# Kernel tuning notes

Hardware: AMD Instinct MI355X
Metric: run time of the kernel (lower is better)

Reference implementation:

```python
import jax, jax.numpy as jnp
import numpy as np

EMBED_DIM = 768
NUM_HEADS = 12
HEAD_DIM = EMBED_DIM // NUM_HEADS
SCALING = HEAD_DIM ** -0.5


def setup_inputs() -> dict:
    key = jax.random.key(0)
    ks = jax.random.split(key, 12)
    B, S, E, H = 4, 1024, EMBED_DIM, NUM_HEADS
    inp = {
        "hidden_states": jax.random.normal(ks[0], (B, S, E), dtype=jnp.float32),
        "pos_row": jax.random.randint(ks[1], (B, S), 0, 64, dtype=jnp.int32),
        "pos_col": jax.random.randint(ks[2], (B, S), 0, 32, dtype=jnp.int32),
        "q_w": jax.random.normal(ks[3], (E, E), dtype=jnp.float32) * 0.02,
        "q_b": jnp.zeros((E,), dtype=jnp.float32),
        "k_w": jax.random.normal(ks[4], (E, E), dtype=jnp.float32) * 0.02,
        "k_b": jnp.zeros((E,), dtype=jnp.float32),
        "v_w": jax.random.normal(ks[5], (E, E), dtype=jnp.float32) * 0.02,
        "v_b": jnp.zeros((E,), dtype=jnp.float32),
        "o_w": jax.random.normal(ks[6], (E, E), dtype=jnp.float32) * 0.02,
        "o_b": jnp.zeros((E,), dtype=jnp.float32),
        "rel_table": jax.random.normal(ks[7], (4, H), dtype=jnp.float32) * 0.02,
    }
    return inp


def _generate_bias(pos_row, pos_col, rel_table):
    # relative row/col differences: [B, S, S]
    rel_row = pos_row[:, :, None] - pos_row[:, None, :]
    rel_col = pos_col[:, :, None] - pos_col[:, None, :]
    rel_cell = jnp.abs(rel_row) + jnp.abs(rel_col)
    # table index: other=0, same row=1, same col=2, same cell=3 (priority order as in torch code)
    idx = jnp.where(rel_row == 0, 1, 0)
    idx = jnp.where(rel_col == 0, 2, idx)
    idx = jnp.where(rel_cell == 0, 3, idx)
    # gather: [B, S, S, H] -> [B, H, S, S]
    bias = rel_table[idx]
    return jnp.transpose(bias, (0, 3, 1, 2))


def reference(hidden_states, pos_row, pos_col, q_w, q_b, k_w, k_b, v_w, v_b, o_w, o_b, rel_table):
    B, S, E = hidden_states.shape
    H, D = NUM_HEADS, HEAD_DIM

    def shape(x):  # [B, S, E] -> [B, H, S, D]
        return jnp.transpose(x.reshape(B, S, H, D), (0, 2, 1, 3))

    q = shape((hidden_states @ q_w.T + q_b) * SCALING)
    k = shape(hidden_states @ k_w.T + k_b)
    v = shape(hidden_states @ v_w.T + v_b)

    # [B, H, S, S]
    attn = jnp.einsum("bhqd,bhkd->bhqk", q, k)
    attn = attn + _generate_bias(pos_row, pos_col, rel_table)
    attn = jax.nn.softmax(attn, axis=-1)

    out = jnp.einsum("bhqk,bhkd->bhqd", attn, v)  # [B, H, S, D]
    out = jnp.transpose(out, (0, 2, 1, 3)).reshape(B, S, E)
    return out @ o_w.T + o_b
```

## Files before the change

### kernel.cpp

```cpp
#include <hip/hip_runtime.h>

#define NHEADS 12
#define HDIM   64
#define EMB    768
#define SEQ    1024
#define BATCH  4
#define MTOT   (BATCH * SEQ)

typedef __bf16 bf16x8 __attribute__((ext_vector_type(8)));
typedef float  f32x4  __attribute__((ext_vector_type(4)));

#define GLB(p) ((const __attribute__((address_space(1))) uint32_t*)(p))
#define LDS(p) ((__attribute__((address_space(3))) uint32_t*)(p))

__device__ __forceinline__ uint bfr(float f) {
    uint u = __float_as_uint(f);
    return (u + 0x7fffu + ((u >> 16) & 1u)) >> 16;
}

__global__ __launch_bounds__(256) void split_f32(
    const float* __restrict__ x, ushort* __restrict__ hi,
    ushort* __restrict__ lo, int n4)
{
    int i = blockIdx.x * 256 + threadIdx.x;
    if (i >= n4) return;
    float4 v = ((const float4*)x)[i];
    float f[4] = {v.x, v.y, v.z, v.w};
    ushort hh[4], ll[4];
#pragma unroll
    for (int j = 0; j < 4; ++j) {
        uint h = bfr(f[j]);
        float hf = __uint_as_float(h << 16);
        ll[j] = (ushort)bfr(f[j] - hf);
        hh[j] = (ushort)h;
    }
    ushort4 hv = {hh[0], hh[1], hh[2], hh[3]};
    ushort4 lv = {ll[0], ll[1], ll[2], ll[3]};
    ((ushort4*)hi)[i] = hv;
    ((ushort4*)lo)[i] = lv;
}

template <int MODE>
__global__ __launch_bounds__(256) void gemm_mfma(
    const ushort* __restrict__ Ah, const ushort* __restrict__ Al,
    const ushort* __restrict__ Wh, const ushort* __restrict__ Wl,
    const float* __restrict__ b0, const float* __restrict__ b1,
    const float* __restrict__ b2,
    ushort* __restrict__ q16, ushort* __restrict__ k16,
    ushort* __restrict__ vT16, float* __restrict__ o0)
{
    __shared__ __align__(16) ushort lds_buf[16384];
    char* ldsc = (char*)lds_buf;

    const int t  = threadIdx.x;
    const int w  = t >> 6;
    const int l  = t & 63;
    const int m0 = blockIdx.x * 128;
    const int n0 = blockIdx.y * 128;
    const int wm = w >> 1;
    const int wn = w & 1;

    const int soff0 = w * 1024 + l * 16;
    const int soff1 = soff0 + 4096;
    const int srow0 = soff0 >> 6, srow1 = soff1 >> 6;
    const int ss0 = (((soff0 >> 4) & 3) ^ ((srow0 >> 1) & 3));
    const int ss1 = (((soff1 >> 4) & 3) ^ ((srow1 >> 1) & 3));

    const char* gb[4] = {
        (const char*)Ah + (size_t)m0 * 1536,
        (const char*)Al + (size_t)m0 * 1536,
        (const char*)Wh + (size_t)n0 * 1536,
        (const char*)Wl + (size_t)n0 * 1536};
    const size_t go0 = (size_t)srow0 * 1536 + ss0 * 16;
    const size_t go1 = (size_t)srow1 * 1536 + ss1 * 16;
    const int ldsu0 = w * 1024;
    const int ldsu1 = w * 1024 + 4096;

    int aoff[4], boff[4];
#pragma unroll
    for (int i = 0; i < 4; ++i) {
        int row = wm * 64 + i * 16 + (l & 15);
        aoff[i] = row * 64 + ((((l >> 4) ^ ((row >> 1) & 3))) << 4);
        int rn = wn * 64 + i * 16 + (l & 15);
        boff[i] = rn * 64 + ((((l >> 4) ^ ((rn >> 1) & 3))) << 4);
    }

    f32x4 acc[4][4] = {};

    for (int ks = 0; ks < 24; ++ks) {
        const size_t kb = (size_t)ks * 64;
        __syncthreads();
#pragma unroll
        for (int tt = 0; tt < 4; ++tt) {
            __builtin_amdgcn_global_load_lds(GLB(gb[tt] + go0 + kb),
                                             LDS(ldsc + tt * 8192 + ldsu0), 16, 0, 0);
            __builtin_amdgcn_global_load_lds(GLB(gb[tt] + go1 + kb),
                                             LDS(ldsc + tt * 8192 + ldsu1), 16, 0, 0);
        }
        __syncthreads();

        bf16x8 ah[4], al[4], bh[4], bl[4];
#pragma unroll
        for (int i = 0; i < 4; ++i) {
            ah[i] = *(const bf16x8*)(ldsc + aoff[i]);
            al[i] = *(const bf16x8*)(ldsc + 8192 + aoff[i]);
            bh[i] = *(const bf16x8*)(ldsc + 16384 + boff[i]);
            bl[i] = *(const bf16x8*)(ldsc + 24576 + boff[i]);
        }
#pragma unroll
        for (int i = 0; i < 4; ++i)
#pragma unroll
            for (int j = 0; j < 4; ++j) {
                acc[i][j] = __builtin_amdgcn_mfma_f32_16x16x32_bf16(ah[i], bh[j], acc[i][j], 0, 0, 0);
                acc[i][j] = __builtin_amdgcn_mfma_f32_16x16x32_bf16(ah[i], bl[j], acc[i][j], 0, 0, 0);
                acc[i][j] = __builtin_amdgcn_mfma_f32_16x16x32_bf16(al[i], bh[j], acc[i][j], 0, 0, 0);
            }
    }

    const int mrow_base = m0 + wm * 64 + ((l >> 4) << 2);

    if (MODE == 1) {
        const int which = (n0 >= 1536) ? 2 : (n0 >= 768 ? 1 : 0);
        const float* bp = (which == 0) ? b0 : (which == 1 ? b1 : b2);
        ushort* op = (which == 0) ? q16 : (which == 1 ? k16 : vT16);
        const float scale = (which == 0) ? 0.125f : 1.0f;
        const int nin_base = n0 - which * 768 + wn * 64 + (l & 15);
#pragma unroll
        for (int j = 0; j < 4; ++j) {
            const int n_in = nin_base + j * 16;
            const float bv = bp[n_in];
            const int h = n_in >> 6, d = n_in & 63;
#pragma unroll
            for (int i = 0; i < 4; ++i)
#pragma unroll
                for (int r = 0; r < 4; ++r) {
                    const int m = mrow_base + i * 16 + r;
                    const int bb = m >> 10, s = m & 1023;
                    const ushort u = (ushort)bfr((acc[i][j][r] + bv) * scale);
                    const size_t dst = (which == 2)
                        ? ((size_t)((bb * NHEADS + h) * HDIM + d) * SEQ + s)
                        : ((size_t)((bb * NHEADS + h) * SEQ + s) * HDIM + d);
                    op[dst] = u;
                }
        }
    } else {
        const int nin_base = n0 + wn * 64 + (l & 15);
#pragma unroll
        for (int j = 0; j < 4; ++j) {
            const int n_in = nin_base + j * 16;
            const float bv = b0[n_in];
#pragma unroll
            for (int i = 0; i < 4; ++i)
#pragma unroll
                for (int r = 0; r < 4; ++r) {
                    const int m = mrow_base + i * 16 + r;
                    o0[(size_t)m * 768 + n_in] = acc[i][j][r] + bv;
                }
        }
    }
}

#define QPOFF  0
#define KOFF   8192
#define VOFF   16384
#define POSOFF 24576

__global__ __launch_bounds__(256) void attn_mfma(
    const ushort* __restrict__ q16, const ushort* __restrict__ k16,
    const ushort* __restrict__ vT16, const int* __restrict__ pos_row,
    const int* __restrict__ pos_col, const float* __restrict__ rel_table,
    ushort* __restrict__ aoh, ushort* __restrict__ aol)
{
    __shared__ __align__(16) char lds[24832];

    const int t  = threadIdx.x;
    const int w  = t >> 6;
    const int l  = t & 63;
    const int bh = blockIdx.y;
    const int b  = bh / NHEADS;
    const int h  = bh - b * NHEADS;
    const int q0g = blockIdx.x * 64;

    const char* qb  = (const char*)(q16 + (size_t)bh * SEQ * HDIM);
    const char* kb  = (const char*)(k16 + (size_t)bh * SEQ * HDIM);
    const char* vtb = (const char*)(vT16 + (size_t)bh * HDIM * SEQ);

    const float t0 = rel_table[0 * NHEADS + h];
    const float t1 = rel_table[1 * NHEADS + h];
    const float t2 = rel_table[2 * NHEADS + h];
    const float t3 = rel_table[3 * NHEADS + h];

    const int o1 = t * 16, o2 = o1 + 4096;
    const int r1 = o1 >> 7, r2 = o2 >> 7;
    const int kq1 = o1 ^ ((r1 & 7) << 4);
    const int kq2 = o2 ^ ((r2 & 7) << 4);
    const int vs1 = r1 * 2048 + (((((o1 >> 4) & 7) ^ (r1 & 7))) << 4);
    const int vs2 = r2 * 2048 + (((((o2 >> 4) & 7) ^ (r2 & 7))) << 4);

    __builtin_amdgcn_global_load_lds(GLB(qb + (size_t)q0g * 128 + kq1),
                                     LDS(lds + QPOFF + w * 1024), 16, 0, 0);
    __builtin_amdgcn_global_load_lds(GLB(qb + (size_t)q0g * 128 + kq2),
                                     LDS(lds + QPOFF + w * 1024 + 4096), 16, 0, 0);

    const int qrow_g = q0g + w * 16 + (l & 15);
    const int pq = (pos_row[b * SEQ + qrow_g] << 8) | pos_col[b * SEQ + qrow_g];

    __syncthreads();

    bf16x8 qf[2];
    const int qrl = w * 16 + (l & 15);
#pragma unroll
    for (int ks = 0; ks < 2; ++ks)
        qf[ks] = *(const bf16x8*)(lds + QPOFF + qrl * 128 +
                                  ((((l >> 4) + 4 * ks) ^ (qrl & 7)) << 4));

    f32x4 pv[4] = {};
    float m_run = -1e30f, l_run = 0.0f;

    const int prow = l & 15;
    const int pswz = (prow & 7) << 4;
    const int pwbase = QPOFF + w * 2048 + prow * 128;

    for (int kt = 0; kt < 16; ++kt) {
        const int k0g = kt * 64;
        __syncthreads();
        __builtin_amdgcn_global_load_lds(GLB(kb + (size_t)k0g * 128 + kq1),
                                         LDS(lds + KOFF + w * 1024), 16, 0, 0);
        __builtin_amdgcn_global_load_lds(GLB(kb + (size_t)k0g * 128 + kq2),
                                         LDS(lds + KOFF + w * 1024 + 4096), 16, 0, 0);
        __builtin_amdgcn_global_load_lds(GLB(vtb + (size_t)k0g * 2 + vs1),
                                         LDS(lds + VOFF + w * 1024), 16, 0, 0);
        __builtin_amdgcn_global_load_lds(GLB(vtb + (size_t)k0g * 2 + vs2),
                                         LDS(lds + VOFF + w * 1024 + 4096), 16, 0, 0);
        if (t < 64) {
            int pr = pos_row[b * SEQ + k0g + t];
            int pc = pos_col[b * SEQ + k0g + t];
            *(int*)(lds + POSOFF + t * 4) = (pr << 8) | pc;
        }
        __syncthreads();

        f32x4 sacc[4] = {};
#pragma unroll
        for (int ks = 0; ks < 2; ++ks) {
            const bf16x8 qq = qf[ks];
#pragma unroll
            for (int j = 0; j < 4; ++j) {
                const int krow = j * 16 + (l & 15);
                const bf16x8 kf = *(const bf16x8*)(lds + KOFF + krow * 128 +
                                                   ((((l >> 4) + 4 * ks) ^ (krow & 7)) << 4));
                sacc[j] = __builtin_amdgcn_mfma_f32_16x16x32_bf16(kf, qq, sacc[j], 0, 0, 0);
            }
        }

        int4 pk4[4];
#pragma unroll
        for (int j = 0; j < 4; ++j)
            pk4[j] = *(const int4*)(lds + POSOFF + (l >> 4) * 16 + j * 64);

        float sv[16];
#pragma unroll
        for (int j = 0; j < 4; ++j) {
            const int pkk[4] = {pk4[j].x, pk4[j].y, pk4[j].z, pk4[j].w};
#pragma unroll
            for (int r = 0; r < 4; ++r) {
                const int dd = pq ^ pkk[r];
                const float bs = ((dd & 0xFF00) == 0)
                                     ? (((dd & 0xFF) == 0) ? t3 : t1)
                                     : (((dd & 0xFF) == 0) ? t2 : t0);
                sv[j * 4 + r] = sacc[j][r] + bs;
            }
        }
        float pm = sv[0];
#pragma unroll
        for (int i = 1; i < 16; ++i) pm = fmaxf(pm, sv[i]);
        pm = fmaxf(pm, __shfl_xor(pm, 16));
        pm = fmaxf(pm, __shfl_xor(pm, 32));
        const float mnew = fmaxf(m_run, pm);
        float psum = 0.0f;
#pragma unroll
        for (int i = 0; i < 16; ++i) {
            sv[i] = __expf(sv[i] - mnew);
            psum += sv[i];
        }
        psum += __shfl_xor(psum, 16);
        psum += __shfl_xor(psum, 32);
        const float alpha = __expf(m_run - mnew);
        l_run = l_run * alpha + psum;
        m_run = mnew;

#pragma unroll
        for (int r = 0; r < 4; ++r) {
            const float ar = __shfl(alpha, (l >> 4) * 4 + r);
#pragma unroll
            for (int i = 0; i < 4; ++i) pv[i][r] *= ar;
        }

#pragma unroll
        for (int j = 0; j < 4; ++j)
#pragma unroll
            for (int p2 = 0; p2 < 2; ++p2) {
                const uint u = bfr(sv[j * 4 + 2 * p2]) | (bfr(sv[j * 4 + 2 * p2 + 1]) << 16);
                const int adr = pwbase + (((l >> 4) * 8 + 4 * p2 + 32 * j) ^ pswz);
                *(uint*)(lds + adr) = u;
            }

#pragma unroll
        for (int ks = 0; ks < 2; ++ks) {
            const bf16x8 pf = *(const bf16x8*)(lds + pwbase +
                                               ((((l >> 4) + 4 * ks) << 4) ^ pswz));
#pragma unroll
            for (int i = 0; i < 4; ++i) {
                const int vrow = i * 16 + (l & 15);
                const bf16x8 vf = *(const bf16x8*)(lds + VOFF + vrow * 128 +
                                                   ((((l >> 4) + 4 * ks) ^ (vrow & 7)) << 4));
                pv[i] = __builtin_amdgcn_mfma_f32_16x16x32_bf16(pf, vf, pv[i], 0, 0, 0);
            }
        }
    }

    const float rinv = 1.0f / l_run;
#pragma unroll
    for (int r = 0; r < 4; ++r) {
        const float inv = __shfl(rinv, (l >> 4) * 4 + r);
        const int mrow = b * SEQ + q0g + w * 16 + (l >> 4) * 4 + r;
        const size_t base = (size_t)mrow * 768 + h * 64 + prow;
#pragma unroll
        for (int i = 0; i < 4; ++i) {
            const float o = pv[i][r] * inv;
            const uint hu = bfr(o);
            const float hf = __uint_as_float(hu << 16);
            const uint lu = bfr(o - hf);
            aoh[base + 16 * i] = (ushort)hu;
            aol[base + 16 * i] = (ushort)lu;
        }
    }
}

extern "C" void kernel_launch(void* const* d_in, const int* in_sizes, int n_in,
                              void* d_out, int out_size, void* d_ws, size_t ws_size,
                              hipStream_t stream)
{
    const float* hs      = (const float*)d_in[0];
    const int*   pos_row = (const int*)d_in[1];
    const int*   pos_col = (const int*)d_in[2];
    const float* q_w     = (const float*)d_in[3];
    const float* q_b     = (const float*)d_in[4];
    const float* k_w     = (const float*)d_in[5];
    const float* k_b     = (const float*)d_in[6];
    const float* v_w     = (const float*)d_in[7];
    const float* v_b     = (const float*)d_in[8];
    const float* o_w     = (const float*)d_in[9];
    const float* o_b     = (const float*)d_in[10];
    const float* rel_tab = (const float*)d_in[11];

    char* ws = (char*)d_ws;
    const size_t HS_N = (size_t)MTOT * EMB;
    const size_t W_N  = (size_t)EMB * EMB;
    ushort* hsh = (ushort*)ws;  ws += HS_N * 2;
    ushort* hsl = (ushort*)ws;  ws += HS_N * 2;
    ushort* wch = (ushort*)ws;  ws += 3 * W_N * 2;
    ushort* wcl = (ushort*)ws;  ws += 3 * W_N * 2;
    ushort* woh = (ushort*)ws;  ws += W_N * 2;
    ushort* wol = (ushort*)ws;  ws += W_N * 2;
    ushort* aoh = (ushort*)ws;  ws += HS_N * 2;
    ushort* aol = (ushort*)ws;  ws += HS_N * 2;
    ushort* q16 = (ushort*)ws;  ws += HS_N * 2;
    ushort* k16 = (ushort*)ws;  ws += HS_N * 2;
    ushort* vT16 = (ushort*)ws; ws += HS_N * 2;

    split_f32<<<(int)(HS_N / 4 / 256), 256, 0, stream>>>(hs, hsh, hsl, (int)(HS_N / 4));
    split_f32<<<(int)(W_N / 4 / 256), 256, 0, stream>>>(q_w, wch, wcl, (int)(W_N / 4));
    split_f32<<<(int)(W_N / 4 / 256), 256, 0, stream>>>(k_w, wch + W_N, wcl + W_N, (int)(W_N / 4));
    split_f32<<<(int)(W_N / 4 / 256), 256, 0, stream>>>(v_w, wch + 2 * W_N, wcl + 2 * W_N, (int)(W_N / 4));
    split_f32<<<(int)(W_N / 4 / 256), 256, 0, stream>>>(o_w, woh, wol, (int)(W_N / 4));

    gemm_mfma<1><<<dim3(MTOT / 128, 2304 / 128), 256, 0, stream>>>(
        hsh, hsl, wch, wcl, q_b, k_b, v_b, q16, k16, vT16, nullptr);

    attn_mfma<<<dim3(SEQ / 64, BATCH * NHEADS), 256, 0, stream>>>(
        q16, k16, vT16, pos_row, pos_col, rel_tab, aoh, aol);

    gemm_mfma<0><<<dim3(MTOT / 128, EMB / 128), 256, 0, stream>>>(
        aoh, aol, woh, wol, o_b, nullptr, nullptr,
        nullptr, nullptr, nullptr, (float*)d_out);
}
```

Before: 243.5 us.

## Double-buffer LDS in GEMM and attention, merge weight splits, shrink output GEMM tile

Adds double-buffered LDS staging to both the projection GEMM and the attention kernel, so the next K or KV tile is loaded while the current one is computed, with one barrier per iteration. Merges the four weight-split launches into a single 2D-grid kernel. Templates the GEMM on BM and uses 64-row tiles for the output projection to launch more blocks. LDS use per block doubles (roughly 64KB in the GEMM and about 41KB in attention), which may lower occupancy.

```diff
diff --git a/kernel.cpp b/kernel.cpp
--- a/kernel.cpp
+++ b/kernel.cpp
@@ -40,7 +40,35 @@
     ((ushort4*)lo)[i] = lv;
 }
 
-template <int MODE>
+__global__ __launch_bounds__(256) void split_w4(
+    const float* __restrict__ w0, const float* __restrict__ w1,
+    const float* __restrict__ w2, const float* __restrict__ w3,
+    ushort* __restrict__ wch, ushort* __restrict__ wcl,
+    ushort* __restrict__ woh, ushort* __restrict__ wol, int n4)
+{
+    const int y = blockIdx.y;
+    const float* src = (y == 0) ? w0 : (y == 1) ? w1 : (y == 2) ? w2 : w3;
+    ushort* hi = (y < 3) ? (wch + (size_t)y * (EMB * EMB)) : woh;
+    ushort* lo = (y < 3) ? (wcl + (size_t)y * (EMB * EMB)) : wol;
+    int i = blockIdx.x * 256 + threadIdx.x;
+    if (i >= n4) return;
+    float4 v = ((const float4*)src)[i];
+    float f[4] = {v.x, v.y, v.z, v.w};
+    ushort hh[4], ll[4];
+#pragma unroll
+    for (int j = 0; j < 4; ++j) {
+        uint h = bfr(f[j]);
+        float hf = __uint_as_float(h << 16);
+        ll[j] = (ushort)bfr(f[j] - hf);
+        hh[j] = (ushort)h;
+    }
+    ushort4 hv = {hh[0], hh[1], hh[2], hh[3]};
+    ushort4 lv = {ll[0], ll[1], ll[2], ll[3]};
+    ((ushort4*)hi)[i] = hv;
+    ((ushort4*)lo)[i] = lv;
+}
+
+template <int MODE, int BM>
 __global__ __launch_bounds__(256) void gemm_mfma(
     const ushort* __restrict__ Ah, const ushort* __restrict__ Al,
     const ushort* __restrict__ Wh, const ushort* __restrict__ Wl,
@@ -49,75 +77,92 @@
     ushort* __restrict__ q16, ushort* __restrict__ k16,
     ushort* __restrict__ vT16, float* __restrict__ o0)
 {
-    __shared__ __align__(16) ushort lds_buf[16384];
-    char* ldsc = (char*)lds_buf;
+    constexpr int SA = BM * 64;
+    constexpr int SB = 8192;
+    constexpr int TS = 2 * SA + 2 * SB;
+    constexpr int MFRAG = BM / 32;
+    constexpr int WMS = BM / 2;
+
+    __shared__ __align__(16) char ldsc[2 * TS];
 
     const int t  = threadIdx.x;
     const int w  = t >> 6;
     const int l  = t & 63;
-    const int m0 = blockIdx.x * 128;
+    const int m0 = blockIdx.x * BM;
     const int n0 = blockIdx.y * 128;
     const int wm = w >> 1;
     const int wn = w & 1;
-
-    const int soff0 = w * 1024 + l * 16;
-    const int soff1 = soff0 + 4096;
-    const int srow0 = soff0 >> 6, srow1 = soff1 >> 6;
-    const int ss0 = (((soff0 >> 4) & 3) ^ ((srow0 >> 1) & 3));
-    const int ss1 = (((soff1 >> 4) & 3) ^ ((srow1 >> 1) & 3));
 
     const char* gb[4] = {
         (const char*)Ah + (size_t)m0 * 1536,
         (const char*)Al + (size_t)m0 * 1536,
         (const char*)Wh + (size_t)n0 * 1536,
         (const char*)Wl + (size_t)n0 * 1536};
-    const size_t go0 = (size_t)srow0 * 1536 + ss0 * 16;
-    const size_t go1 = (size_t)srow1 * 1536 + ss1 * 16;
-    const int ldsu0 = w * 1024;
-    const int ldsu1 = w * 1024 + 4096;
-
-    int aoff[4], boff[4];
+
+    int aoff[MFRAG], boff[4];
+#pragma unroll
+    for (int i = 0; i < MFRAG; ++i) {
+        int row = wm * WMS + i * 16 + (l & 15);
+        aoff[i] = row * 64 + ((((l >> 4) ^ ((row >> 1) & 3))) << 4);
+    }
 #pragma unroll
     for (int i = 0; i < 4; ++i) {
-        int row = wm * 64 + i * 16 + (l & 15);
-        aoff[i] = row * 64 + ((((l >> 4) ^ ((row >> 1) & 3))) << 4);
         int rn = wn * 64 + i * 16 + (l & 15);
         boff[i] = rn * 64 + ((((l >> 4) ^ ((rn >> 1) & 3))) << 4);
     }
 
-    f32x4 acc[4][4] = {};
+    auto stage = [&](int ks, int buf) {
+        const size_t kb = (size_t)ks * 64;
+        char* dst = ldsc + buf * TS;
+#pragma unroll
+        for (int tt = 0; tt < 4; ++tt) {
+            const int tsz  = (tt < 2) ? SA : SB;
+            const int tbas = (tt == 0) ? 0 : (tt == 1) ? SA : (tt == 2) ? 2 * SA : 2 * SA + SB;
+#pragma unroll
+            for (int p = 0; p < tsz; p += 4096) {
+                const int soff = p + w * 1024 + l * 16;
+                const int srow = soff >> 6;
+                const int slot = (soff >> 4) & 3;
+                const size_t go = (size_t)srow * 1536 +
+                                  ((slot ^ ((srow >> 1) & 3)) << 4) + kb;
+                __builtin_amdgcn_global_load_lds(GLB(gb[tt] + go),
+                                                 LDS(dst + tbas + p + w * 1024), 16, 0, 0);
+            }
+        }
+    };
+
+    f32x4 acc[MFRAG][4] = {};
+
+    stage(0, 0);
+    __syncthreads();
 
     for (int ks = 0; ks < 24; ++ks) {
-        const size_t kb = (size_t)ks * 64;
-        __syncthreads();
-#pragma unroll
-        for (int tt = 0; tt < 4; ++tt) {
-            __builtin_amdgcn_global_load_lds(GLB(gb[tt] + go0 + kb),
-                                             LDS(ldsc + tt * 8192 + ldsu0), 16, 0, 0);
-            __builtin_amdgcn_global_load_lds(GLB(gb[tt] + go1 + kb),
-                                             LDS(ldsc + tt * 8192 + ldsu1), 16, 0, 0);
-        }
-        __syncthreads();
-
-        bf16x8 ah[4], al[4], bh[4], bl[4];
+        if (ks + 1 < 24) stage(ks + 1, (ks + 1) & 1);
+
+        const char* cur = ldsc + (ks & 1) * TS;
+        bf16x8 ah[MFRAG], al[MFRAG], bh[4], bl[4];
+#pragma unroll
+        for (int i = 0; i < MFRAG; ++i) {
+            ah[i] = *(const bf16x8*)(cur + aoff[i]);
+            al[i] = *(const bf16x8*)(cur + SA + aoff[i]);
+        }
 #pragma unroll
         for (int i = 0; i < 4; ++i) {
-            ah[i] = *(const bf16x8*)(ldsc + aoff[i]);
-            al[i] = *(const bf16x8*)(ldsc + 8192 + aoff[i]);
-            bh[i] = *(const bf16x8*)(ldsc + 16384 + boff[i]);
-            bl[i] = *(const bf16x8*)(ldsc + 24576 + boff[i]);
-        }
-#pragma unroll
-        for (int i = 0; i < 4; ++i)
+            bh[i] = *(const bf16x8*)(cur + 2 * SA + boff[i]);
+            bl[i] = *(const bf16x8*)(cur + 2 * SA + SB + boff[i]);
+        }
+#pragma unroll
+        for (int i = 0; i < MFRAG; ++i)
 #pragma unroll
             for (int j = 0; j < 4; ++j) {
                 acc[i][j] = __builtin_amdgcn_mfma_f32_16x16x32_bf16(ah[i], bh[j], acc[i][j], 0, 0, 0);
                 acc[i][j] = __builtin_amdgcn_mfma_f32_16x16x32_bf16(ah[i], bl[j], acc[i][j], 0, 0, 0);
                 acc[i][j] = __builtin_amdgcn_mfma_f32_16x16x32_bf16(al[i], bh[j], acc[i][j], 0, 0, 0);
             }
-    }
-
-    const int mrow_base = m0 + wm * 64 + ((l >> 4) << 2);
+        __syncthreads();
+    }
+
+    const int mrow_base = m0 + wm * WMS + ((l >> 4) << 2);
 
     if (MODE == 1) {
         const int which = (n0 >= 1536) ? 2 : (n0 >= 768 ? 1 : 0);
@@ -131,7 +176,7 @@
             const float bv = bp[n_in];
             const int h = n_in >> 6, d = n_in & 63;
 #pragma unroll
-            for (int i = 0; i < 4; ++i)
+            for (int i = 0; i < MFRAG; ++i)
 #pragma unroll
                 for (int r = 0; r < 4; ++r) {
                     const int m = mrow_base + i * 16 + r;
@@ -150,7 +195,7 @@
             const int n_in = nin_base + j * 16;
             const float bv = b0[n_in];
 #pragma unroll
-            for (int i = 0; i < 4; ++i)
+            for (int i = 0; i < MFRAG; ++i)
 #pragma unroll
                 for (int r = 0; r < 4; ++r) {
                     const int m = mrow_base + i * 16 + r;
@@ -162,8 +207,8 @@
 
 #define QPOFF  0
 #define KOFF   8192
-#define VOFF   16384
-#define POSOFF 24576
+#define VOFF   24576
+#define POSOFF 40960
 
 __global__ __launch_bounds__(256) void attn_mfma(
     const ushort* __restrict__ q16, const ushort* __restrict__ k16,
@@ -171,7 +216,7 @@
     const int* __restrict__ pos_col, const float* __restrict__ rel_table,
     ushort* __restrict__ aoh, ushort* __restrict__ aol)
 {
-    __shared__ __align__(16) char lds[24832];
+    __shared__ __align__(16) char lds[41472];
 
     const int t  = threadIdx.x;
     const int w  = t >> 6;
@@ -197,10 +242,28 @@
     const int vs1 = r1 * 2048 + (((((o1 >> 4) & 7) ^ (r1 & 7))) << 4);
     const int vs2 = r2 * 2048 + (((((o2 >> 4) & 7) ^ (r2 & 7))) << 4);
 
+    auto stage_kv = [&](int kt, int buf) {
+        const int k0g = kt * 64;
+        __builtin_amdgcn_global_load_lds(GLB(kb + (size_t)k0g * 128 + kq1),
+                                         LDS(lds + KOFF + buf * 8192 + w * 1024), 16, 0, 0);
+        __builtin_amdgcn_global_load_lds(GLB(kb + (size_t)k0g * 128 + kq2),
+                                         LDS(lds + KOFF + buf * 8192 + w * 1024 + 4096), 16, 0, 0);
+        __builtin_amdgcn_global_load_lds(GLB(vtb + (size_t)k0g * 2 + vs1),
+                                         LDS(lds + VOFF + buf * 8192 + w * 1024), 16, 0, 0);
+        __builtin_amdgcn_global_load_lds(GLB(vtb + (size_t)k0g * 2 + vs2),
+                                         LDS(lds + VOFF + buf * 8192 + w * 1024 + 4096), 16, 0, 0);
+        if (t < 64) {
+            int pr = pos_row[b * SEQ + k0g + t];
+            int pc = pos_col[b * SEQ + k0g + t];
+            *(int*)(lds + POSOFF + buf * 256 + t * 4) = (pr << 8) | pc;
+        }
+    };
+
     __builtin_amdgcn_global_load_lds(GLB(qb + (size_t)q0g * 128 + kq1),
                                      LDS(lds + QPOFF + w * 1024), 16, 0, 0);
     __builtin_amdgcn_global_load_lds(GLB(qb + (size_t)q0g * 128 + kq2),
                                      LDS(lds + QPOFF + w * 1024 + 4096), 16, 0, 0);
+    stage_kv(0, 0);
 
     const int qrow_g = q0g + w * 16 + (l & 15);
     const int pq = (pos_row[b * SEQ + qrow_g] << 8) | pos_col[b * SEQ + qrow_g];
@@ -222,22 +285,11 @@
     const int pwbase = QPOFF + w * 2048 + prow * 128;
 
     for (int kt = 0; kt < 16; ++kt) {
-        const int k0g = kt * 64;
-        __syncthreads();
-        __builtin_amdgcn_global_load_lds(GLB(kb + (size_t)k0g * 128 + kq1),
-                                         LDS(lds + KOFF + w * 1024), 16, 0, 0);
-        __builtin_amdgcn_global_load_lds(GLB(kb + (size_t)k0g * 128 + kq2),
-                                         LDS(lds + KOFF + w * 1024 + 4096), 16, 0, 0);
-        __builtin_amdgcn_global_load_lds(GLB(vtb + (size_t)k0g * 2 + vs1),
-                                         LDS(lds + VOFF + w * 1024), 16, 0, 0);
-        __builtin_amdgcn_global_load_lds(GLB(vtb + (size_t)k0g * 2 + vs2),
-                                         LDS(lds + VOFF + w * 1024 + 4096), 16, 0, 0);
-        if (t < 64) {
-            int pr = pos_row[b * SEQ + k0g + t];
-            int pc = pos_col[b * SEQ + k0g + t];
-            *(int*)(lds + POSOFF + t * 4) = (pr << 8) | pc;
-        }
-        __syncthreads();
+        const int cb = kt & 1;
+        if (kt + 1 < 16) stage_kv(kt + 1, cb ^ 1);
+        const char* kbuf = lds + KOFF + cb * 8192;
+        const char* vbuf = lds + VOFF + cb * 8192;
+        const char* pbuf = lds + POSOFF + cb * 256;
 
         f32x4 sacc[4] = {};
 #pragma unroll
@@ -246,7 +298,7 @@
 #pragma unroll
             for (int j = 0; j < 4; ++j) {
                 const int krow = j * 16 + (l & 15);
-                const bf16x8 kf = *(const bf16x8*)(lds + KOFF + krow * 128 +
+                const bf16x8 kf = *(const bf16x8*)(kbuf + krow * 128 +
                                                    ((((l >> 4) + 4 * ks) ^ (krow & 7)) << 4));
                 sacc[j] = __builtin_amdgcn_mfma_f32_16x16x32_bf16(kf, qq, sacc[j], 0, 0, 0);
             }
@@ -255,7 +307,7 @@
         int4 pk4[4];
 #pragma unroll
         for (int j = 0; j < 4; ++j)
-            pk4[j] = *(const int4*)(lds + POSOFF + (l >> 4) * 16 + j * 64);
+            pk4[j] = *(const int4*)(pbuf + (l >> 4) * 16 + j * 64);
 
         float sv[16];
 #pragma unroll
@@ -311,11 +363,12 @@
 #pragma unroll
             for (int i = 0; i < 4; ++i) {
                 const int vrow = i * 16 + (l & 15);
-                const bf16x8 vf = *(const bf16x8*)(lds + VOFF + vrow * 128 +
+                const bf16x8 vf = *(const bf16x8*)(vbuf + vrow * 128 +
                                                    ((((l >> 4) + 4 * ks) ^ (vrow & 7)) << 4));
                 pv[i] = __builtin_amdgcn_mfma_f32_16x16x32_bf16(pf, vf, pv[i], 0, 0, 0);
             }
         }
+        __syncthreads();
     }
 
     const float rinv = 1.0f / l_run;
@@ -369,18 +422,16 @@
     ushort* vT16 = (ushort*)ws; ws += HS_N * 2;
 
     split_f32<<<(int)(HS_N / 4 / 256), 256, 0, stream>>>(hs, hsh, hsl, (int)(HS_N / 4));
-    split_f32<<<(int)(W_N / 4 / 256), 256, 0, stream>>>(q_w, wch, wcl, (int)(W_N / 4));
-    split_f32<<<(int)(W_N / 4 / 256), 256, 0, stream>>>(k_w, wch + W_N, wcl + W_N, (int)(W_N / 4));
-    split_f32<<<(int)(W_N / 4 / 256), 256, 0, stream>>>(v_w, wch + 2 * W_N, wcl + 2 * W_N, (int)(W_N / 4));
-    split_f32<<<(int)(W_N / 4 / 256), 256, 0, stream>>>(o_w, woh, wol, (int)(W_N / 4));
-
-    gemm_mfma<1><<<dim3(MTOT / 128, 2304 / 128), 256, 0, stream>>>(
+    split_w4<<<dim3((int)(W_N / 4 / 256), 4), 256, 0, stream>>>(
+        q_w, k_w, v_w, o_w, wch, wcl, woh, wol, (int)(W_N / 4));
+
+    gemm_mfma<1, 128><<<dim3(MTOT / 128, 2304 / 128), 256, 0, stream>>>(
         hsh, hsl, wch, wcl, q_b, k_b, v_b, q16, k16, vT16, nullptr);
 
     attn_mfma<<<dim3(SEQ / 64, BATCH * NHEADS), 256, 0, stream>>>(
         q16, k16, vT16, pos_row, pos_col, rel_tab, aoh, aol);
 
-    gemm_mfma<0><<<dim3(MTOT / 128, EMB / 128), 256, 0, stream>>>(
+    gemm_mfma<0, 64><<<dim3(MTOT / 64, EMB / 128), 256, 0, stream>>>(
         aoh, aol, woh, wol, o_b, nullptr, nullptr,
         nullptr, nullptr, nullptr, (float*)d_out);
 }
```

Result: faster. 229.7 us (-5.7%).
